# Kernel tuning notes

Hardware: AMD Instinct MI355X
Metric: run time of the kernel (lower is better)

Reference implementation:

```python
import jax, jax.numpy as jnp
import numpy as np

E, H, D, T, K = 8, 1024, 2048, 4096, 2


def setup_inputs() -> dict:
    key = jax.random.key(0)
    k1, k2, k3, k4, k5, k6 = jax.random.split(key, 6)
    hidden_states = jax.random.normal(k1, (T, H), dtype=jnp.float32)
    topk_weights = jax.random.uniform(k2, (T, K), dtype=jnp.float32)
    topk_ids = jax.random.randint(k3, (T, K), 0, E, dtype=jnp.int32)
    std = 0.01  # nnx.initializers.normal() default stddev
    wi_0 = std * jax.random.normal(k4, (E, H, D), dtype=jnp.float32)
    wi_1 = std * jax.random.normal(k5, (E, H, D), dtype=jnp.float32)
    wo = std * jax.random.normal(k6, (E, D, H), dtype=jnp.float32)
    return {
        "hidden_states": hidden_states,
        "topk_weights": topk_weights,
        "topk_ids": topk_ids,
        "wi_0": wi_0,
        "wi_1": wi_1,
        "wo": wo,
    }


def reference(hidden_states, topk_weights, topk_ids, wi_0, wi_1, wo):
    num_experts = wi_0.shape[0]
    inputs_flat = hidden_states  # [T, H] (already 2D)
    num_tokens = inputs_flat.shape[0]
    # Scatter top-k routing weights into a dense [T, E] combine matrix
    expert_weights = jnp.zeros((num_tokens, num_experts), dtype=inputs_flat.dtype)
    token_idx = jnp.arange(num_tokens)[:, None]
    expert_weights = expert_weights.at[token_idx, topk_ids].set(topk_weights)
    # Dense all-experts SwiGLU FFN
    layer_w0 = jnp.einsum("th,ehd->ted", inputs_flat, wi_0)
    layer_w1 = jnp.einsum("th,ehd->ted", inputs_flat, wi_1)
    activated = jax.nn.silu(layer_w0) * layer_w1  # [T, E, D]
    expert_outputs = jnp.einsum("ted,edh->teh", activated, wo)
    final_output = jnp.einsum("te,teh->th", expert_weights, expert_outputs)
    return final_output.reshape(hidden_states.shape)
```

## Files before the change

### kernel.cpp

```cpp
#include <hip/hip_runtime.h>
#include <hip/hip_bf16.h>
#include <stdint.h>

#define NEXP 8
#define HDIM 1024
#define DDIM 2048
#define NTOK 4096
#define MAXROWS (NTOK * 2)

typedef __attribute__((ext_vector_type(8))) short bf16x8;
typedef __attribute__((ext_vector_type(4))) float f32x4;

#define OFF_META 0
#define OFF_BASE 64
#define OFF_ATOK 256
#define OFF_SLOT (OFF_ATOK + MAXROWS * 4)
#define OFF_TOKW (OFF_SLOT + NTOK * 2 * 4)
#define OFF_ABF  ((size_t)1 << 20)
#define OFF_ACT  (OFF_ABF + (size_t)MAXROWS * HDIM * 2)
#define OFF_Y    (OFF_ACT + (size_t)MAXROWS * DDIM * 2)
#define OFF_W0B  (OFF_Y   + (size_t)MAXROWS * HDIM * 2)
#define OFF_W1B  (OFF_W0B + (size_t)NEXP * HDIM * DDIM * 2)
#define OFF_WOB  (OFF_W1B + (size_t)NEXP * HDIM * DDIM * 2)
#define WS_NEED  (OFF_WOB + (size_t)NEXP * DDIM * HDIM * 2)

__device__ __forceinline__ unsigned short f2b(float f) {
  __hip_bfloat16 h = __float2bfloat16(f);
  union { __hip_bfloat16 h; unsigned short u; } c; c.h = h; return c.u;
}
__device__ __forceinline__ float b2f(unsigned short u) {
  unsigned int x = ((unsigned int)u) << 16;
  float f; __builtin_memcpy(&f, &x, 4); return f;
}
__device__ __forceinline__ void gload_lds16(const void* g, void* l) {
  __builtin_amdgcn_global_load_lds(
      (const __attribute__((address_space(1))) unsigned int*)g,
      (__attribute__((address_space(3))) unsigned int*)l, 16, 0, 0);
}

__global__ __launch_bounds__(256) void k_cvtw(const float* __restrict__ src,
                                              unsigned short* __restrict__ dst,
                                              int n4) {
  int i = blockIdx.x * 256 + threadIdx.x;
  const int stride = gridDim.x * 256;
  for (; i < n4; i += stride) {
    const float4 v = ((const float4*)src)[i];
    ushort4 o;
    o.x = f2b(v.x); o.y = f2b(v.y); o.z = f2b(v.z); o.w = f2b(v.w);
    ((ushort4*)dst)[i] = o;
  }
}

__global__ __launch_bounds__(256) void k_route(
    const int* __restrict__ ids, const float* __restrict__ tw,
    int* __restrict__ meta, int* __restrict__ base,
    int* __restrict__ assignTok, int* __restrict__ tokSlot,
    float* __restrict__ tokW) {
  __shared__ int cnt[NEXP];
  __shared__ int cur[NEXP];
  __shared__ int sbase[NEXP + 1];
  const int tid = threadIdx.x;
  if (tid < NEXP) cnt[tid] = 0;
  __syncthreads();
  for (int t = tid; t < NTOK; t += 256) {
    const int e0 = ids[t * 2], e1 = ids[t * 2 + 1];
    if (e0 != e1) atomicAdd(&cnt[e0], 1);
    atomicAdd(&cnt[e1], 1);
  }
  __syncthreads();
  if (tid == 0) {
    int s = 0;
    for (int e = 0; e < NEXP; e++) { sbase[e] = s; s += cnt[e]; }
    sbase[NEXP] = s;
    meta[0] = s;
    for (int e = 0; e <= NEXP; e++) base[e] = sbase[e];
  }
  if (tid < NEXP) cur[tid] = 0;
  __syncthreads();
  for (int t = tid; t < NTOK; t += 256) {
    const int e0 = ids[t * 2], e1 = ids[t * 2 + 1];
    int r0 = -1;
    if (e0 != e1) { r0 = sbase[e0] + atomicAdd(&cur[e0], 1); assignTok[r0] = t; }
    const int r1 = sbase[e1] + atomicAdd(&cur[e1], 1);
    assignTok[r1] = t;
    tokSlot[t * 2] = r0; tokSlot[t * 2 + 1] = r1;
    tokW[t * 2] = tw[t * 2]; tokW[t * 2 + 1] = tw[t * 2 + 1];
  }
}

__global__ __launch_bounds__(256) void k_gather(
    const float* __restrict__ hidden, const int* __restrict__ meta,
    const int* __restrict__ assignTok, unsigned short* __restrict__ Abf) {
  const int r = blockIdx.x;
  if (r >= meta[0]) return;
  const int t = assignTok[r];
  const int tid = threadIdx.x;
  const float4 v = *(const float4*)(hidden + (size_t)t * HDIM + tid * 4);
  ushort4 o;
  o.x = f2b(v.x); o.y = f2b(v.y); o.z = f2b(v.z); o.w = f2b(v.w);
  *(ushort4*)(Abf + (size_t)r * HDIM + tid * 4) = o;
}

__device__ __forceinline__ int swz_off(int row, int chunk) {
  return row * 64 + (((chunk) ^ (row & 7)) << 3);
}
__device__ __forceinline__ int cswz(int row, int col) {
  return row * 128 + ((((col >> 3) ^ (row & 15))) << 3) + (col & 7);
}

__device__ __forceinline__ void loadBtile(const unsigned short* __restrict__ W,
                                          int ldw, int k0, int nb, int kb,
                                          bf16x8 (&o)[4]) {
#pragma unroll
  for (int kk = 0; kk < 8; kk++) {
    const ushort4 v = *(const ushort4*)(W + (size_t)(k0 + kb + kk) * ldw + nb);
    o[0][kk] = (short)v.x; o[1][kk] = (short)v.y;
    o[2][kk] = (short)v.z; o[3][kk] = (short)v.w;
  }
}
__device__ __forceinline__ void loadBtile(const float* __restrict__ W,
                                          int ldw, int k0, int nb, int kb,
                                          bf16x8 (&o)[4]) {
#pragma unroll
  for (int kk = 0; kk < 8; kk++) {
    const float4 v = *(const float4*)(W + (size_t)(k0 + kb + kk) * ldw + nb);
    o[0][kk] = (short)f2b(v.x); o[1][kk] = (short)f2b(v.y);
    o[2][kk] = (short)f2b(v.z); o[3][kk] = (short)f2b(v.w);
  }
}
__device__ __forceinline__ void storeBtile(unsigned short* __restrict__ Bl,
                                           int nb, int kb, const bf16x8 (&o)[4]) {
  const int cin = kb >> 3;
  *(bf16x8*)(Bl + swz_off(nb + 0, cin)) = o[0];
  *(bf16x8*)(Bl + swz_off(nb + 1, cin)) = o[1];
  *(bf16x8*)(Bl + swz_off(nb + 2, cin)) = o[2];
  *(bf16x8*)(Bl + swz_off(nb + 3, cin)) = o[3];
}

template <typename WT>
__global__ __launch_bounds__(256, 2) void k_gemm_up(
    const unsigned short* __restrict__ Abf, const WT* __restrict__ wi0,
    const WT* __restrict__ wi1, const int* __restrict__ base,
    unsigned short* __restrict__ act) {
  const int bid = blockIdx.x;
  const int gg = bid >> 8, mt = (bid >> 3) & 31, r8 = bid & 7;
  const int g = gg * 8 + r8;
  const int e = g >> 4, nt = g & 15;
  const int rbase = base[e], rend = base[e + 1];
  const int ne = rend - rbase;
  if (mt * 128 >= ne) return;

  __shared__ __align__(16) unsigned short lds[24576];
  unsigned short* Al = lds;
  unsigned short* Bg = lds + 8192;
  unsigned short* Bu = lds + 16384;

  const int tid = threadIdx.x;
  const int wv = tid >> 6, l = tid & 63;
  const int wm = wv >> 1, wn = wv & 1;
  const WT* W0 = wi0 + (size_t)e * HDIM * DDIM + nt * 128;
  const WT* W1 = wi1 + (size_t)e * HDIM * DDIM + nt * 128;
  const int nb = (tid & 31) * 4, kb = (tid >> 5) * 8;

  f32x4 accg[4][4], accu[4][4];
#pragma unroll
  for (int i = 0; i < 4; i++)
#pragma unroll
    for (int j = 0; j < 4; j++) {
      accg[i][j] = {0.f, 0.f, 0.f, 0.f};
      accu[i][j] = {0.f, 0.f, 0.f, 0.f};
    }

  bf16x8 pg[4], pu[4];
  loadBtile(W0, DDIM, 0, nb, kb, pg);
  loadBtile(W1, DDIM, 0, nb, kb, pu);

  for (int k0 = 0; k0 < HDIM; k0 += 64) {
    __syncthreads();
    storeBtile(Bg, nb, kb, pg);
    storeBtile(Bu, nb, kb, pu);
#pragma unroll
    for (int q = 0; q < 4; q++) {
      const int rowt = (wv * 4 + q) * 8 + (l >> 3);
      const int j = l & 7;
      int rr = rbase + mt * 128 + rowt;
      if (rr >= rend) rr = rend - 1;
      const unsigned short* gs =
          Abf + (size_t)rr * HDIM + k0 + ((j ^ (rowt & 7)) << 3);
      gload_lds16(gs, Al + (wv * 4 + q) * 512);
    }
    __syncthreads();
    if (k0 + 64 < HDIM) {
      loadBtile(W0, DDIM, k0 + 64, nb, kb, pg);
      loadBtile(W1, DDIM, k0 + 64, nb, kb, pu);
    }
#pragma unroll
    for (int kk = 0; kk < 2; kk++) {
      bf16x8 af[4], bg[4], bu[4];
#pragma unroll
      for (int mi = 0; mi < 4; mi++) {
        const int row = wm * 64 + mi * 16 + (l & 15);
        af[mi] = *(const bf16x8*)(Al + swz_off(row, kk * 4 + (l >> 4)));
      }
#pragma unroll
      for (int ni = 0; ni < 4; ni++) {
        const int row = wn * 64 + ni * 16 + (l & 15);
        const int off = swz_off(row, kk * 4 + (l >> 4));
        bg[ni] = *(const bf16x8*)(Bg + off);
        bu[ni] = *(const bf16x8*)(Bu + off);
      }
#pragma unroll
      for (int mi = 0; mi < 4; mi++)
#pragma unroll
        for (int ni = 0; ni < 4; ni++) {
          accg[mi][ni] = __builtin_amdgcn_mfma_f32_16x16x32_bf16(
              af[mi], bg[ni], accg[mi][ni], 0, 0, 0);
          accu[mi][ni] = __builtin_amdgcn_mfma_f32_16x16x32_bf16(
              af[mi], bu[ni], accu[mi][ni], 0, 0, 0);
        }
    }
  }
  __syncthreads();
  unsigned short* Cl = lds;
#pragma unroll
  for (int mi = 0; mi < 4; mi++)
#pragma unroll
    for (int ni = 0; ni < 4; ni++) {
      const int col = wn * 64 + ni * 16 + (l & 15);
#pragma unroll
      for (int rr = 0; rr < 4; rr++) {
        const int row = wm * 64 + mi * 16 + (l >> 4) * 4 + rr;
        const float gv = accg[mi][ni][rr];
        const float uv = accu[mi][ni][rr];
        const float a = (gv / (1.f + __expf(-gv))) * uv;
        Cl[cswz(row, col)] = f2b(a);
      }
    }
  __syncthreads();
  {
    const int row = tid >> 1, half = tid & 1;
    const int rw = rbase + mt * 128 + row;
    if (rw < rend) {
      unsigned short* dst = act + (size_t)rw * DDIM + nt * 128 + half * 64;
#pragma unroll
      for (int q = 0; q < 8; q++) {
        const int c = half * 8 + q;
        *(bf16x8*)(dst + q * 8) =
            *(const bf16x8*)(Cl + row * 128 + ((c ^ (row & 15)) << 3));
      }
    }
  }
}

template <typename WT>
__global__ __launch_bounds__(256, 2) void k_gemm_down(
    const unsigned short* __restrict__ act, const WT* __restrict__ wo,
    const int* __restrict__ base, unsigned short* __restrict__ Y) {
  const int bid = blockIdx.x;
  const int gg = bid >> 8, mt = (bid >> 3) & 31, r8 = bid & 7;
  const int g = gg * 8 + r8;
  const int e = g >> 3, nt = g & 7;
  const int rbase = base[e], rend = base[e + 1];
  const int ne = rend - rbase;
  if (mt * 128 >= ne) return;

  __shared__ __align__(16) unsigned short lds[16384];
  unsigned short* Al = lds;
  unsigned short* Bw = lds + 8192;

  const int tid = threadIdx.x;
  const int wv = tid >> 6, l = tid & 63;
  const int wm = wv >> 1, wn = wv & 1;
  const WT* W = wo + (size_t)e * DDIM * HDIM + nt * 128;
  const int nb = (tid & 31) * 4, kb = (tid >> 5) * 8;

  f32x4 acc[4][4];
#pragma unroll
  for (int i = 0; i < 4; i++)
#pragma unroll
    for (int j = 0; j < 4; j++) acc[i][j] = {0.f, 0.f, 0.f, 0.f};

  bf16x8 pw[4];
  loadBtile(W, HDIM, 0, nb, kb, pw);

  for (int k0 = 0; k0 < DDIM; k0 += 64) {
    __syncthreads();
    storeBtile(Bw, nb, kb, pw);
#pragma unroll
    for (int q = 0; q < 4; q++) {
      const int rowt = (wv * 4 + q) * 8 + (l >> 3);
      const int j = l & 7;
      int rr = rbase + mt * 128 + rowt;
      if (rr >= rend) rr = rend - 1;
      const unsigned short* gs =
          act + (size_t)rr * DDIM + k0 + ((j ^ (rowt & 7)) << 3);
      gload_lds16(gs, Al + (wv * 4 + q) * 512);
    }
    __syncthreads();
    if (k0 + 64 < DDIM) loadBtile(W, HDIM, k0 + 64, nb, kb, pw);
#pragma unroll
    for (int kk = 0; kk < 2; kk++) {
      bf16x8 af[4], bw[4];
#pragma unroll
      for (int mi = 0; mi < 4; mi++) {
        const int row = wm * 64 + mi * 16 + (l & 15);
        af[mi] = *(const bf16x8*)(Al + swz_off(row, kk * 4 + (l >> 4)));
      }
#pragma unroll
      for (int ni = 0; ni < 4; ni++) {
        const int row = wn * 64 + ni * 16 + (l & 15);
        bw[ni] = *(const bf16x8*)(Bw + swz_off(row, kk * 4 + (l >> 4)));
      }
#pragma unroll
      for (int mi = 0; mi < 4; mi++)
#pragma unroll
        for (int ni = 0; ni < 4; ni++)
          acc[mi][ni] = __builtin_amdgcn_mfma_f32_16x16x32_bf16(
              af[mi], bw[ni], acc[mi][ni], 0, 0, 0);
    }
  }
  __syncthreads();
  unsigned short* Cl = lds;
#pragma unroll
  for (int mi = 0; mi < 4; mi++)
#pragma unroll
    for (int ni = 0; ni < 4; ni++) {
      const int col = wn * 64 + ni * 16 + (l & 15);
#pragma unroll
      for (int rr = 0; rr < 4; rr++) {
        const int row = wm * 64 + mi * 16 + (l >> 4) * 4 + rr;
        Cl[cswz(row, col)] = f2b(acc[mi][ni][rr]);
      }
    }
  __syncthreads();
  {
    const int row = tid >> 1, half = tid & 1;
    const int rw = rbase + mt * 128 + row;
    if (rw < rend) {
      unsigned short* dst = Y + (size_t)rw * HDIM + nt * 128 + half * 64;
#pragma unroll
      for (int q = 0; q < 8; q++) {
        const int c = half * 8 + q;
        *(bf16x8*)(dst + q * 8) =
            *(const bf16x8*)(Cl + row * 128 + ((c ^ (row & 15)) << 3));
      }
    }
  }
}

__global__ __launch_bounds__(256) void k_combine(
    const unsigned short* __restrict__ Y, const int* __restrict__ tokSlot,
    const float* __restrict__ tokW, float* __restrict__ out) {
  const int t = blockIdx.x;
  const int tid = threadIdx.x;
  int r0 = tokSlot[t * 2];
  const int r1 = tokSlot[t * 2 + 1];
  float w0 = tokW[t * 2];
  const float w1 = tokW[t * 2 + 1];
  if (r0 < 0) { w0 = 0.f; r0 = r1; }
  const ushort4 a = *(const ushort4*)(Y + (size_t)r0 * HDIM + tid * 4);
  const ushort4 b = *(const ushort4*)(Y + (size_t)r1 * HDIM + tid * 4);
  float4 o;
  o.x = w0 * b2f(a.x) + w1 * b2f(b.x);
  o.y = w0 * b2f(a.y) + w1 * b2f(b.y);
  o.z = w0 * b2f(a.z) + w1 * b2f(b.z);
  o.w = w0 * b2f(a.w) + w1 * b2f(b.w);
  *(float4*)(out + (size_t)t * HDIM + tid * 4) = o;
}

extern "C" void kernel_launch(void* const* d_in, const int* in_sizes, int n_in,
                              void* d_out, int out_size, void* d_ws,
                              size_t ws_size, hipStream_t stream) {
  const float* hidden = (const float*)d_in[0];
  const float* tw = (const float*)d_in[1];
  const int* ids = (const int*)d_in[2];
  const float* wi0 = (const float*)d_in[3];
  const float* wi1 = (const float*)d_in[4];
  const float* wo = (const float*)d_in[5];
  float* out = (float*)d_out;
  char* ws = (char*)d_ws;

  int* meta = (int*)(ws + OFF_META);
  int* base = (int*)(ws + OFF_BASE);
  int* assignTok = (int*)(ws + OFF_ATOK);
  int* tokSlot = (int*)(ws + OFF_SLOT);
  float* tokW = (float*)(ws + OFF_TOKW);
  unsigned short* Abf = (unsigned short*)(ws + OFF_ABF);
  unsigned short* act = (unsigned short*)(ws + OFF_ACT);
  unsigned short* Y = (unsigned short*)(ws + OFF_Y);

  k_route<<<dim3(1), dim3(256), 0, stream>>>(ids, tw, meta, base, assignTok,
                                             tokSlot, tokW);
  k_gather<<<dim3(MAXROWS), dim3(256), 0, stream>>>(hidden, meta, assignTok,
                                                    Abf);
  if (ws_size >= WS_NEED) {
    unsigned short* W0b = (unsigned short*)(ws + OFF_W0B);
    unsigned short* W1b = (unsigned short*)(ws + OFF_W1B);
    unsigned short* Wob = (unsigned short*)(ws + OFF_WOB);
    const int n4 = NEXP * HDIM * DDIM / 4;
    k_cvtw<<<dim3(2048), dim3(256), 0, stream>>>(wi0, W0b, n4);
    k_cvtw<<<dim3(2048), dim3(256), 0, stream>>>(wi1, W1b, n4);
    k_cvtw<<<dim3(2048), dim3(256), 0, stream>>>(wo, Wob, n4);
    k_gemm_up<unsigned short><<<dim3(4096), dim3(256), 0, stream>>>(
        Abf, W0b, W1b, base, act);
    k_gemm_down<unsigned short><<<dim3(2048), dim3(256), 0, stream>>>(
        act, Wob, base, Y);
  } else {
    k_gemm_up<float><<<dim3(4096), dim3(256), 0, stream>>>(Abf, wi0, wi1, base,
                                                           act);
    k_gemm_down<float><<<dim3(2048), dim3(256), 0, stream>>>(act, wo, base, Y);
  }
  k_combine<<<dim3(NTOK), dim3(256), 0, stream>>>(Y, tokSlot, tokW, out);
}
```

Measured before the change: 465.1 us.

## Double-buffer A tiles in MoE GEMMs, fuse weight conversion launches

Both grouped GEMMs now double-buffer the A tile in LDS, issuing the next tile's async global-to-LDS loads and B register loads before computing on the current tile. Plain __syncthreads calls are replaced with explicit waitcnt/barrier asm, and the MFMA section is wrapped in s_setprio. The LDS swizzle changes to XOR row with row>>2. The three weight-conversion kernels are merged into one launch using a 2D grid. The goal is to hide global load latency behind MFMA work, at the cost of more LDS per block (64 KB for up), which may lower occupancy.

```diff
diff --git a/kernel.cpp b/kernel.cpp
--- a/kernel.cpp
+++ b/kernel.cpp
@@ -24,6 +24,10 @@
 #define OFF_WOB  (OFF_W1B + (size_t)NEXP * HDIM * DDIM * 2)
 #define WS_NEED  (OFF_WOB + (size_t)NEXP * DDIM * HDIM * 2)
 
+#define BAR_LGKM() asm volatile("s_waitcnt lgkmcnt(0)\ns_barrier" ::: "memory")
+#define BAR_FULL() \
+  asm volatile("s_waitcnt vmcnt(0) lgkmcnt(0)\ns_barrier" ::: "memory")
+
 __device__ __forceinline__ unsigned short f2b(float f) {
   __hip_bfloat16 h = __float2bfloat16(f);
   union { __hip_bfloat16 h; unsigned short u; } c; c.h = h; return c.u;
@@ -38,9 +42,12 @@
       (__attribute__((address_space(3))) unsigned int*)l, 16, 0, 0);
 }
 
-__global__ __launch_bounds__(256) void k_cvtw(const float* __restrict__ src,
-                                              unsigned short* __restrict__ dst,
-                                              int n4) {
+__global__ __launch_bounds__(256) void k_cvtw3(
+    const float* __restrict__ s0, const float* __restrict__ s1,
+    const float* __restrict__ s2, unsigned short* __restrict__ d0,
+    unsigned short* __restrict__ d1, unsigned short* __restrict__ d2, int n4) {
+  const float* src = blockIdx.y == 0 ? s0 : (blockIdx.y == 1 ? s1 : s2);
+  unsigned short* dst = blockIdx.y == 0 ? d0 : (blockIdx.y == 1 ? d1 : d2);
   int i = blockIdx.x * 256 + threadIdx.x;
   const int stride = gridDim.x * 256;
   for (; i < n4; i += stride) {
@@ -101,8 +108,9 @@
   *(ushort4*)(Abf + (size_t)r * HDIM + tid * 4) = o;
 }
 
+__device__ __forceinline__ int swz_q(int row) { return (row ^ (row >> 2)) & 7; }
 __device__ __forceinline__ int swz_off(int row, int chunk) {
-  return row * 64 + (((chunk) ^ (row & 7)) << 3);
+  return row * 64 + ((chunk ^ swz_q(row)) << 3);
 }
 __device__ __forceinline__ int cswz(int row, int col) {
   return row * 128 + ((((col >> 3) ^ (row & 15))) << 3) + (col & 7);
@@ -128,8 +136,8 @@
     o[2][kk] = (short)f2b(v.z); o[3][kk] = (short)f2b(v.w);
   }
 }
-__device__ __forceinline__ void storeBtile(unsigned short* __restrict__ Bl,
-                                           int nb, int kb, const bf16x8 (&o)[4]) {
+__device__ __forceinline__ void storeBtile(unsigned short* Bl, int nb, int kb,
+                                           const bf16x8 (&o)[4]) {
   const int cin = kb >> 3;
   *(bf16x8*)(Bl + swz_off(nb + 0, cin)) = o[0];
   *(bf16x8*)(Bl + swz_off(nb + 1, cin)) = o[1];
@@ -150,10 +158,9 @@
   const int ne = rend - rbase;
   if (mt * 128 >= ne) return;
 
-  __shared__ __align__(16) unsigned short lds[24576];
-  unsigned short* Al = lds;
-  unsigned short* Bg = lds + 8192;
-  unsigned short* Bu = lds + 16384;
+  __shared__ __align__(16) unsigned short lds[32768];
+  unsigned short* Bg = lds + 16384;
+  unsigned short* Bu = lds + 24576;
 
   const int tid = threadIdx.x;
   const int wv = tid >> 6, l = tid & 63;
@@ -172,28 +179,39 @@
     }
 
   bf16x8 pg[4], pu[4];
+#pragma unroll
+  for (int q = 0; q < 4; q++) {
+    const int rowt = (wv * 4 + q) * 8 + (l >> 3);
+    int rr = rbase + mt * 128 + rowt;
+    if (rr >= rend) rr = rend - 1;
+    gload_lds16(Abf + (size_t)rr * HDIM + (((l & 7) ^ swz_q(rowt)) << 3),
+                lds + (wv * 4 + q) * 512);
+  }
   loadBtile(W0, DDIM, 0, nb, kb, pg);
   loadBtile(W1, DDIM, 0, nb, kb, pu);
-
-  for (int k0 = 0; k0 < HDIM; k0 += 64) {
-    __syncthreads();
-    storeBtile(Bg, nb, kb, pg);
-    storeBtile(Bu, nb, kb, pu);
-#pragma unroll
-    for (int q = 0; q < 4; q++) {
-      const int rowt = (wv * 4 + q) * 8 + (l >> 3);
-      const int j = l & 7;
-      int rr = rbase + mt * 128 + rowt;
-      if (rr >= rend) rr = rend - 1;
-      const unsigned short* gs =
-          Abf + (size_t)rr * HDIM + k0 + ((j ^ (rowt & 7)) << 3);
-      gload_lds16(gs, Al + (wv * 4 + q) * 512);
-    }
-    __syncthreads();
-    if (k0 + 64 < HDIM) {
-      loadBtile(W0, DDIM, k0 + 64, nb, kb, pg);
-      loadBtile(W1, DDIM, k0 + 64, nb, kb, pu);
-    }
+  storeBtile(Bg, nb, kb, pg);
+  storeBtile(Bu, nb, kb, pu);
+  BAR_FULL();
+
+  int cur = 0;
+  for (int t = 0; t < 16; ++t) {
+    if (t + 1 < 16) {
+      const int k1 = (t + 1) * 64;
+      const int noff = (cur ^ 1) * 8192;
+#pragma unroll
+      for (int q = 0; q < 4; q++) {
+        const int rowt = (wv * 4 + q) * 8 + (l >> 3);
+        int rr = rbase + mt * 128 + rowt;
+        if (rr >= rend) rr = rend - 1;
+        gload_lds16(Abf + (size_t)rr * HDIM + k1 +
+                        (((l & 7) ^ swz_q(rowt)) << 3),
+                    lds + noff + (wv * 4 + q) * 512);
+      }
+      loadBtile(W0, DDIM, k1, nb, kb, pg);
+      loadBtile(W1, DDIM, k1, nb, kb, pu);
+    }
+    const unsigned short* Al = lds + cur * 8192;
+    __builtin_amdgcn_s_setprio(1);
 #pragma unroll
     for (int kk = 0; kk < 2; kk++) {
       bf16x8 af[4], bg[4], bu[4];
@@ -219,8 +237,15 @@
               af[mi], bu[ni], accu[mi][ni], 0, 0, 0);
         }
     }
-  }
-  __syncthreads();
+    __builtin_amdgcn_s_setprio(0);
+    BAR_LGKM();
+    if (t + 1 < 16) {
+      storeBtile(Bg, nb, kb, pg);
+      storeBtile(Bu, nb, kb, pu);
+    }
+    BAR_FULL();
+    cur ^= 1;
+  }
   unsigned short* Cl = lds;
 #pragma unroll
   for (int mi = 0; mi < 4; mi++)
@@ -264,9 +289,8 @@
   const int ne = rend - rbase;
   if (mt * 128 >= ne) return;
 
-  __shared__ __align__(16) unsigned short lds[16384];
-  unsigned short* Al = lds;
-  unsigned short* Bw = lds + 8192;
+  __shared__ __align__(16) unsigned short lds[24576];
+  unsigned short* Bw = lds + 16384;
 
   const int tid = threadIdx.x;
   const int wv = tid >> 6, l = tid & 63;
@@ -281,23 +305,36 @@
     for (int j = 0; j < 4; j++) acc[i][j] = {0.f, 0.f, 0.f, 0.f};
 
   bf16x8 pw[4];
+#pragma unroll
+  for (int q = 0; q < 4; q++) {
+    const int rowt = (wv * 4 + q) * 8 + (l >> 3);
+    int rr = rbase + mt * 128 + rowt;
+    if (rr >= rend) rr = rend - 1;
+    gload_lds16(act + (size_t)rr * DDIM + (((l & 7) ^ swz_q(rowt)) << 3),
+                lds + (wv * 4 + q) * 512);
+  }
   loadBtile(W, HDIM, 0, nb, kb, pw);
-
-  for (int k0 = 0; k0 < DDIM; k0 += 64) {
-    __syncthreads();
-    storeBtile(Bw, nb, kb, pw);
-#pragma unroll
-    for (int q = 0; q < 4; q++) {
-      const int rowt = (wv * 4 + q) * 8 + (l >> 3);
-      const int j = l & 7;
-      int rr = rbase + mt * 128 + rowt;
-      if (rr >= rend) rr = rend - 1;
-      const unsigned short* gs =
-          act + (size_t)rr * DDIM + k0 + ((j ^ (rowt & 7)) << 3);
-      gload_lds16(gs, Al + (wv * 4 + q) * 512);
-    }
-    __syncthreads();
-    if (k0 + 64 < DDIM) loadBtile(W, HDIM, k0 + 64, nb, kb, pw);
+  storeBtile(Bw, nb, kb, pw);
+  BAR_FULL();
+
+  int cur = 0;
+  for (int t = 0; t < 32; ++t) {
+    if (t + 1 < 32) {
+      const int k1 = (t + 1) * 64;
+      const int noff = (cur ^ 1) * 8192;
+#pragma unroll
+      for (int q = 0; q < 4; q++) {
+        const int rowt = (wv * 4 + q) * 8 + (l >> 3);
+        int rr = rbase + mt * 128 + rowt;
+        if (rr >= rend) rr = rend - 1;
+        gload_lds16(act + (size_t)rr * DDIM + k1 +
+                        (((l & 7) ^ swz_q(rowt)) << 3),
+                    lds + noff + (wv * 4 + q) * 512);
+      }
+      loadBtile(W, HDIM, k1, nb, kb, pw);
+    }
+    const unsigned short* Al = lds + cur * 8192;
+    __builtin_amdgcn_s_setprio(1);
 #pragma unroll
     for (int kk = 0; kk < 2; kk++) {
       bf16x8 af[4], bw[4];
@@ -318,8 +355,12 @@
           acc[mi][ni] = __builtin_amdgcn_mfma_f32_16x16x32_bf16(
               af[mi], bw[ni], acc[mi][ni], 0, 0, 0);
     }
-  }
-  __syncthreads();
+    __builtin_amdgcn_s_setprio(0);
+    BAR_LGKM();
+    if (t + 1 < 32) storeBtile(Bw, nb, kb, pw);
+    BAR_FULL();
+    cur ^= 1;
+  }
   unsigned short* Cl = lds;
 #pragma unroll
   for (int mi = 0; mi < 4; mi++)
@@ -398,9 +439,8 @@
     unsigned short* W1b = (unsigned short*)(ws + OFF_W1B);
     unsigned short* Wob = (unsigned short*)(ws + OFF_WOB);
     const int n4 = NEXP * HDIM * DDIM / 4;
-    k_cvtw<<<dim3(2048), dim3(256), 0, stream>>>(wi0, W0b, n4);
-    k_cvtw<<<dim3(2048), dim3(256), 0, stream>>>(wi1, W1b, n4);
-    k_cvtw<<<dim3(2048), dim3(256), 0, stream>>>(wo, Wob, n4);
+    k_cvtw3<<<dim3(2048, 3), dim3(256), 0, stream>>>(wi0, wi1, wo, W0b, W1b,
+                                                     Wob, n4);
     k_gemm_up<unsigned short><<<dim3(4096), dim3(256), 0, stream>>>(
         Abf, W0b, W1b, base, act);
     k_gemm_down<unsigned short><<<dim3(2048), dim3(256), 0, stream>>>(
```

Measured after the change: 430.5 us. 7.4% less time.
